# Performance work log

Measured on AMD Instinct MI355X. Metric: run time of the kernel, lower is better.

The kernel has to match this reference:

```python
import jax, jax.numpy as jnp
import numpy as np

B, N, NEV, E, D, L = 4, 20000, 100000, 400000, 64, 3

def setup_inputs() -> dict:
    key = jax.random.key(0)
    ks = jax.random.split(key, 12)
    x = jax.random.normal(ks[0], (B, N, 3), dtype=jnp.float32)
    # channel 0 is the susceptible boolean mask (0/1)
    mask0 = (jax.random.uniform(ks[1], (B, N)) < 0.3).astype(jnp.float32)
    x = x.at[..., 0].set(mask0)
    dag_edge_index = jax.random.randint(ks[2], (2, E), 0, NEV, dtype=jnp.int64)
    event_to_node = jax.random.randint(ks[3], (NEV,), 0, N, dtype=jnp.int64)
    event_src_node = jax.random.randint(ks[4], (NEV,), 0, N, dtype=jnp.int64)
    s = 1.0 / np.sqrt(D)
    Wp = jax.random.normal(ks[5], (6, D), dtype=jnp.float32) * (1.0 / np.sqrt(6))
    bp = jnp.zeros((D,), dtype=jnp.float32)
    Ws = jax.random.normal(ks[6], (L, D, D), dtype=jnp.float32) * s
    Wa = jax.random.normal(ks[7], (L, D, D), dtype=jnp.float32) * s
    ba = jnp.zeros((L, D), dtype=jnp.float32)
    Wo = jax.random.normal(ks[8], (D,), dtype=jnp.float32) * s
    bo = jnp.zeros((), dtype=jnp.float32)
    return {"x": x, "Wp": Wp, "bp": bp, "Ws": Ws, "Wa": Wa, "ba": ba,
            "Wo": Wo, "bo": bo, "dag_edge_index": dag_edge_index,
            "event_to_node": event_to_node, "event_src_node": event_src_node}

def reference(x, Wp, bp, Ws, Wa, ba, Wo, bo, dag_edge_index, event_to_node, event_src_node):
    n_events = event_src_node.shape[0]
    # event features: [B, n_events, 6] -> project -> ReLU
    ev_feat = jnp.concatenate([x[:, event_src_node, :], x[:, event_to_node, :]], axis=-1)
    h = jax.nn.relu(ev_feat @ Wp + bp)  # [B, n_events, D]
    # reversed DAG edges: src = dag[1], dst = dag[0]
    src_e, dst_e = dag_edge_index[1], dag_edge_index[0]
    deg = jnp.zeros((n_events,), h.dtype).at[dst_e].add(1.0)
    deg = jnp.maximum(deg, 1.0)[None, :, None]
    for l in range(Ws.shape[0]):
        agg = jnp.zeros_like(h).at[:, dst_e].add(h[:, src_e])  # scatter-add mean agg
        h = jax.nn.relu(h @ Ws[l] + (agg / deg) @ Wa[l] + ba[l])
    # aggregate events back to nodes (mean)
    node_emb = jnp.zeros((x.shape[0], x.shape[1], h.shape[-1]), h.dtype).at[:, event_to_node].add(h)
    count = jnp.zeros((x.shape[1],), h.dtype).at[event_to_node].add(1.0)
    node_emb = node_emb / jnp.maximum(count, 1.0)[None, :, None]
    scores = node_emb @ Wo + bo  # [B, N]
    susceptible = x[..., 0] > 0
    scores = jnp.where(susceptible, -jnp.inf, scores)
    return jax.nn.log_softmax(scores, axis=-1)
```

## Files before the change

kernel.cpp:

```cpp
#include <hip/hip_runtime.h>
#include <hip/hip_bf16.h>
#include <math.h>

constexpr int B   = 4;
constexpr int N   = 20000;
constexpr int NEV = 100000;
constexpr int E   = 400000;
constexpr int D   = 64;
constexpr int L   = 3;
constexpr int XS  = 136;
constexpr int CAP = 32;
constexpr int CHUNK = 625;

typedef short  short8 __attribute__((ext_vector_type(8)));
typedef float  f32x4  __attribute__((ext_vector_type(4)));
typedef float  f32x2  __attribute__((ext_vector_type(2)));


__device__ inline unsigned short f2bu(float f) {
  union { __hip_bfloat16 b; unsigned short s; } u;
  u.b = __float2bfloat16(f);
  return u.s;
}
__device__ inline unsigned packbf(float lo, float hi) {
  return ((unsigned)f2bu(hi) << 16) | (unsigned)f2bu(lo);
}


__global__ void k_zero(float4* __restrict__ p, int n4) {
  int i = blockIdx.x * blockDim.x + threadIdx.x;
  if (i < n4) p[i] = make_float4(0.f, 0.f, 0.f, 0.f);
}

__global__ void k_prep(const int* __restrict__ dag,
                       int* __restrict__ cnt,
                       int* __restrict__ csrc,
                       const int* __restrict__ e2n,
                       int* __restrict__ ncount,
                       const float* __restrict__ Ws,
                       const float* __restrict__ Wa,
                       unsigned short* __restrict__ Wt) {
  int bid = blockIdx.x;
  if (bid < 1563) {
    int i = bid * 256 + threadIdx.x;
    if (i < E) {
      int dst = dag[i];
      int src = dag[E + i];
      int pos = atomicAdd(&cnt[dst], 1);
      if (pos < CAP) csrc[dst * CAP + pos] = src;
    }
  } else if (bid < 1954) {
    int i = (bid - 1563) * 256 + threadIdx.x;
    if (i < NEV) atomicAdd(&ncount[e2n[i]], 1);
  } else {
    int i = (bid - 1954) * 256 + threadIdx.x;
    int l = i >> 13;
    int r = i & 8191;
    int n = r >> 7;
    int s = r & 127;
    int sl = (s < 64) ? s : s - 64;
    int c  = (sl & 3) * 16 + (sl >> 2);
    float v = (s < 64) ? Ws[l * 4096 + c * 64 + n]
                       : Wa[l * 4096 + c * 64 + n];
    Wt[l * 8192 + n * 128 + s] = f2bu(v);
  }
}

__global__ __launch_bounds__(256) void k_proj(const float* __restrict__ x,
                                              const float* __restrict__ Wp,
                                              const float* __restrict__ bp,
                                              const int* __restrict__ esrc,
                                              const int* __restrict__ e2n,
                                              unsigned* __restrict__ h,
                                              float* __restrict__ nscore) {
  int gid = blockIdx.x * blockDim.x + threadIdx.x;
  if (gid < B * N) nscore[gid] = 0.f;
  int p   = gid & 15;
  int row = gid >> 4;
  int e   = row >> 2;
  int b   = row & 3;
  int sn = esrc[e], tn = e2n[e];
  const float* xs = x + (size_t)(b * N + sn) * 3;
  const float* xt = x + (size_t)(b * N + tn) * 3;
  float xv[6] = {xs[0], xs[1], xs[2], xt[0], xt[1], xt[2]};
  float a[4];
#pragma unroll
  for (int t = 0; t < 4; ++t) {
    int d = p + 16 * t;
    float acc = bp[d];
#pragma unroll
    for (int k = 0; k < 6; ++k) acc += xv[k] * Wp[k * 64 + d];
    a[t] = fmaxf(acc, 0.f);
  }
  int w = __builtin_amdgcn_cvt_pk_fp8_f32(a[0], a[1], 0, false);
  w     = __builtin_amdgcn_cvt_pk_fp8_f32(a[2], a[3], w, true);
  h[row * 16 + p] = (unsigned)w;
}

template <bool LAST>
__global__ __launch_bounds__(256, 8) void k_layer(
    const unsigned short* __restrict__ Wt,
    const float* __restrict__ ba,
    const float* __restrict__ Wo,
    const int* __restrict__ e2n,
    const int* __restrict__ cnt,
    const int* __restrict__ csrc,
    const unsigned char* __restrict__ h_in,
    unsigned char* __restrict__ h_out,
    float* __restrict__ nscore) {
  __shared__ unsigned short sX[64 * XS];
  const int tid  = threadIdx.x;
  const int wv   = tid >> 6, lane = tid & 63;
  const int e0   = blockIdx.x * 16;
  const int r0   = e0 * 4;

  const int qg = lane >> 4, sub = lane & 15;
  int vidx = csrc[(size_t)(e0 + wv * 4 + qg) * CAP + sub];
  int c_l  = cnt[e0 + wv * 4 + (lane & 3)];

  {
    uint4 v = *(const uint4*)(h_in + (size_t)r0 * 64 + tid * 16);
    int row = tid >> 2, ch = tid & 3;
    unsigned vv[4] = {v.x, v.y, v.z, v.w};
    unsigned out[8];
#pragma unroll
    for (int i = 0; i < 4; ++i) {
      f32x2 lo = __builtin_amdgcn_cvt_pk_f32_fp8((int)vv[i], false);
      f32x2 hi = __builtin_amdgcn_cvt_pk_f32_fp8((int)vv[i], true);
      out[2 * i]     = packbf(lo[0], lo[1]);
      out[2 * i + 1] = packbf(hi[0], hi[1]);
    }
    unsigned short* dst = sX + row * XS + ch * 16;
    *(uint4*)dst       = *(uint4*)&out[0];
    *(uint4*)(dst + 8) = *(uint4*)&out[4];
  }

#pragma unroll
  for (int ei = 0; ei < 4; ++ei) {
    int c = __shfl(c_l, ei, 64);
    int cc16 = min(c, 16);
    float a0 = 0.f, a1 = 0.f, a2 = 0.f, a3 = 0.f;
    int j = 0;
    for (; j + 3 < cc16; j += 4) {
      int s0 = __shfl(vidx, ei * 16 + j + 0, 64);
      int s1 = __shfl(vidx, ei * 16 + j + 1, 64);
      int s2 = __shfl(vidx, ei * 16 + j + 2, 64);
      int s3 = __shfl(vidx, ei * 16 + j + 3, 64);
      unsigned v0 = *(const unsigned*)(h_in + (size_t)s0 * 256 + lane * 4);
      unsigned v1 = *(const unsigned*)(h_in + (size_t)s1 * 256 + lane * 4);
      unsigned v2 = *(const unsigned*)(h_in + (size_t)s2 * 256 + lane * 4);
      unsigned v3 = *(const unsigned*)(h_in + (size_t)s3 * 256 + lane * 4);
      f32x2 l0 = __builtin_amdgcn_cvt_pk_f32_fp8((int)v0, false);
      f32x2 h0 = __builtin_amdgcn_cvt_pk_f32_fp8((int)v0, true);
      f32x2 l1 = __builtin_amdgcn_cvt_pk_f32_fp8((int)v1, false);
      f32x2 h1 = __builtin_amdgcn_cvt_pk_f32_fp8((int)v1, true);
      f32x2 l2 = __builtin_amdgcn_cvt_pk_f32_fp8((int)v2, false);
      f32x2 h2 = __builtin_amdgcn_cvt_pk_f32_fp8((int)v2, true);
      f32x2 l3 = __builtin_amdgcn_cvt_pk_f32_fp8((int)v3, false);
      f32x2 h3 = __builtin_amdgcn_cvt_pk_f32_fp8((int)v3, true);
      a0 += l0[0] + l1[0] + l2[0] + l3[0];
      a1 += l0[1] + l1[1] + l2[1] + l3[1];
      a2 += h0[0] + h1[0] + h2[0] + h3[0];
      a3 += h0[1] + h1[1] + h2[1] + h3[1];
    }
    for (; j < cc16; ++j) {
      int s = __shfl(vidx, ei * 16 + j, 64);
      unsigned v = *(const unsigned*)(h_in + (size_t)s * 256 + lane * 4);
      f32x2 lo = __builtin_amdgcn_cvt_pk_f32_fp8((int)v, false);
      f32x2 hi = __builtin_amdgcn_cvt_pk_f32_fp8((int)v, true);
      a0 += lo[0]; a1 += lo[1]; a2 += hi[0]; a3 += hi[1];
    }
    int cc = min(c, CAP);
    for (int j2 = 16; j2 < cc; ++j2) {
      int s = csrc[(size_t)(e0 + wv * 4 + ei) * CAP + j2];
      unsigned v = *(const unsigned*)(h_in + (size_t)s * 256 + lane * 4);
      f32x2 lo = __builtin_amdgcn_cvt_pk_f32_fp8((int)v, false);
      f32x2 hi = __builtin_amdgcn_cvt_pk_f32_fp8((int)v, true);
      a0 += lo[0]; a1 += lo[1]; a2 += hi[0]; a3 += hi[1];
    }
    float inv = 1.f / fmaxf((float)c, 1.f);
    int lrow = (wv * 4 + ei) * 4 + qg;
    uint2 w;
    w.x = packbf(a0 * inv, a1 * inv);
    w.y = packbf(a2 * inv, a3 * inv);
    *(uint2*)(sX + lrow * XS + 64 + sub * 4) = w;
  }
  __syncthreads();

  const int m = lane & 15, q = lane >> 4;
  f32x4 acc[4];
#pragma unroll
  for (int t = 0; t < 4; ++t) {
    float bv = ba[t * 16 + m];
    acc[t] = (f32x4){bv, bv, bv, bv};
  }
  const unsigned short* xbase = sX + (wv * 16 + m) * XS + q * 8;
  const unsigned short* wbase = Wt + m * 128 + q * 8;
#pragma unroll
  for (int kk = 0; kk < 4; ++kk) {
    short8 av = *(const short8*)(xbase + kk * 32);
#pragma unroll
    for (int t = 0; t < 4; ++t) {
      short8 bv = *(const short8*)(wbase + t * 2048 + kk * 32);
      acc[t] = __builtin_amdgcn_mfma_f32_16x16x32_bf16(av, bv, acc[t], 0, 0, 0);
    }
  }

  if constexpr (!LAST) {
#pragma unroll
    for (int r = 0; r < 4; ++r) {
      int w = __builtin_amdgcn_cvt_pk_fp8_f32(fmaxf(acc[0][r], 0.f),
                                              fmaxf(acc[1][r], 0.f), 0, false);
      w     = __builtin_amdgcn_cvt_pk_fp8_f32(fmaxf(acc[2][r], 0.f),
                                              fmaxf(acc[3][r], 0.f), w, true);
      int grow = r0 + wv * 16 + q * 4 + r;
      ((unsigned*)h_out)[grow * 16 + m] = (unsigned)w;
    }
  } else {
    float w0 = Wo[m], w1 = Wo[16 + m], w2 = Wo[32 + m], w3 = Wo[48 + m];
#pragma unroll
    for (int r = 0; r < 4; ++r) {
      float v = fmaxf(acc[0][r], 0.f) * w0 + fmaxf(acc[1][r], 0.f) * w1
              + fmaxf(acc[2][r], 0.f) * w2 + fmaxf(acc[3][r], 0.f) * w3;
      v += __shfl_xor(v, 1, 64);
      v += __shfl_xor(v, 2, 64);
      v += __shfl_xor(v, 4, 64);
      v += __shfl_xor(v, 8, 64);
      if (m == 0) {
        int grow = r0 + wv * 16 + q * 4 + r;
        int e = grow >> 2, b = grow & 3;
        atomicAdd(&nscore[b * N + e2n[e]], v);
      }
    }
  }
}

__device__ inline float ls_score(const float* nscore, const int* ncount,
                                 const float* x, float bov, int b, int n) {
  return (x[(size_t)(b * N + n) * 3] > 0.f)
             ? -INFINITY
             : nscore[b * N + n] / fmaxf((float)ncount[n], 1.f) + bov;
}

__global__ __launch_bounds__(256) void k_ls1(const float* __restrict__ nscore,
                                             const int* __restrict__ ncount,
                                             const float* __restrict__ x,
                                             const float* __restrict__ bo,
                                             float* __restrict__ pmax,
                                             float* __restrict__ psum) {
  const int b = blockIdx.x >> 5, ch = blockIdx.x & 31;
  const int n0 = ch * CHUNK;
  const int tid = threadIdx.x;
  const float bov = bo[0];
  float s0 = -INFINITY, s1 = -INFINITY, s2 = -INFINITY;
  if (tid < CHUNK)       s0 = ls_score(nscore, ncount, x, bov, b, n0 + tid);
  if (tid + 256 < CHUNK) s1 = ls_score(nscore, ncount, x, bov, b, n0 + tid + 256);
  if (tid + 512 < CHUNK) s2 = ls_score(nscore, ncount, x, bov, b, n0 + tid + 512);
  float m = fmaxf(fmaxf(s0, s1), s2);
  __shared__ float red[4];
#pragma unroll
  for (int o = 32; o; o >>= 1) m = fmaxf(m, __shfl_xor(m, o, 64));
  if ((tid & 63) == 0) red[tid >> 6] = m;
  __syncthreads();
  float pm = fmaxf(fmaxf(red[0], red[1]), fmaxf(red[2], red[3]));
  float pm2 = (pm == -INFINITY) ? 0.f : pm;
  float e = expf(s0 - pm2) + expf(s1 - pm2) + expf(s2 - pm2);
#pragma unroll
  for (int o = 32; o; o >>= 1) e += __shfl_xor(e, o, 64);
  __syncthreads();
  if ((tid & 63) == 0) red[tid >> 6] = e;
  __syncthreads();
  if (tid == 0) {
    pmax[blockIdx.x] = pm;
    psum[blockIdx.x] = red[0] + red[1] + red[2] + red[3];
  }
}

__global__ __launch_bounds__(256) void k_ls3(const float* __restrict__ pmax,
                                             const float* __restrict__ psum,
                                             const float* __restrict__ nscore,
                                             const int* __restrict__ ncount,
                                             const float* __restrict__ x,
                                             const float* __restrict__ bo,
                                             float* __restrict__ out) {
  const int b = blockIdx.x >> 5, ch = blockIdx.x & 31;
  const int n0 = ch * CHUNK;
  const int tid = threadIdx.x;
  const float bov = bo[0];
  __shared__ float sgm, slse;
  if (tid < 64) {
    float pm = (tid < 32) ? pmax[b * 32 + tid] : -INFINITY;
    float ps = (tid < 32) ? psum[b * 32 + tid] : 0.f;
    float gm = pm;
#pragma unroll
    for (int o = 32; o; o >>= 1) gm = fmaxf(gm, __shfl_xor(gm, o, 64));
    float gm2 = (gm == -INFINITY) ? 0.f : gm;
    float c = (pm == -INFINITY) ? 0.f : ps * expf(pm - gm2);
#pragma unroll
    for (int o = 32; o; o >>= 1) c += __shfl_xor(c, o, 64);
    if (tid == 0) { sgm = gm; slse = logf(c); }
  }
  __syncthreads();
  const float gm = sgm, lse = slse;
  for (int i = tid; i < CHUNK; i += 256) {
    int n = n0 + i;
    float s = ls_score(nscore, ncount, x, bov, b, n);
    out[b * N + n] = fmaxf(s - gm - lse, -3.0e38f);
  }
}

extern "C" void kernel_launch(void* const* d_in, const int* in_sizes, int n_in,
                              void* d_out, int out_size, void* d_ws, size_t ws_size,
                              hipStream_t stream) {
  const float* x   = (const float*)d_in[0];
  const float* Wp  = (const float*)d_in[1];
  const float* bp  = (const float*)d_in[2];
  const float* Ws  = (const float*)d_in[3];
  const float* Wa  = (const float*)d_in[4];
  const float* ba  = (const float*)d_in[5];
  const float* Wo  = (const float*)d_in[6];
  const float* bo  = (const float*)d_in[7];
  const int*   dag = (const int*)d_in[8];
  const int*   e2n = (const int*)d_in[9];
  const int*   esr = (const int*)d_in[10];

  int*   ws     = (int*)d_ws;
  int*   cnt    = ws;
  int*   ncount = ws + 100000;
  float* nscore = (float*)(ws + 120000);
  float* pmax   = (float*)(ws + 200000);
  float* psum   = (float*)(ws + 200128);
  int*   csrc   = ws + 200704;
  unsigned short* Wt = (unsigned short*)(ws + 3400704);
  unsigned char* h0 = (unsigned char*)(ws + 3406912);
  unsigned char* h1 = h0 + (size_t)B * NEV * D;
  float* out    = (float*)d_out;

  k_zero<<<(30000 + 255) / 256, 256, 0, stream>>>((float4*)ws, 30000);
  k_prep<<<2050, 256, 0, stream>>>(dag, cnt, csrc, e2n, ncount, Ws, Wa, Wt);
  k_proj<<<(B * NEV * 16) / 256, 256, 0, stream>>>(x, Wp, bp, esr, e2n,
                                                   (unsigned*)h0, nscore);

  k_layer<false><<<NEV / 16, 256, 0, stream>>>(Wt,         ba,       Wo, e2n,
                                               cnt, csrc, h0, h1, nscore);
  k_layer<false><<<NEV / 16, 256, 0, stream>>>(Wt + 8192,  ba + D,   Wo, e2n,
                                               cnt, csrc, h1, h0, nscore);
  k_layer<true><<<NEV / 16, 256, 0, stream>>>(Wt + 16384,  ba + 2*D, Wo, e2n,
                                              cnt, csrc, h0, h1, nscore);

  k_ls1<<<B * 32, 256, 0, stream>>>(nscore, ncount, x, bo, pmax, psum);
  k_ls3<<<B * 32, 256, 0, stream>>>(pmax, psum, nscore, ncount, x, bo, out);
}
```

Measured before the change: 344.3 us.

## Batch neighbor gathers into register buffer and share event inputs via shuffles

In the layer kernel, the neighbor aggregation now issues all up-to-16 fp8 row gathers into a register buffer before any conversion or accumulation, so more loads are in flight at once instead of four at a time. In the projection kernel, each wavefront handles one event across all four batches: 24 lanes load the six input features per batch and broadcast them with shuffles, which removes redundant per-thread index and x loads. The risks are higher register pressure from the 16-entry buffer under launch_bounds(256,8), and predicated unrolled code.

```diff
diff --git a/kernel.cpp b/kernel.cpp
--- a/kernel.cpp
+++ b/kernel.cpp
@@ -75,14 +75,19 @@
                                               float* __restrict__ nscore) {
   int gid = blockIdx.x * blockDim.x + threadIdx.x;
   if (gid < B * N) nscore[gid] = 0.f;
-  int p   = gid & 15;
-  int row = gid >> 4;
-  int e   = row >> 2;
-  int b   = row & 3;
+  const int lane = threadIdx.x & 63;
+  const int e    = gid >> 6;
   int sn = esrc[e], tn = e2n[e];
-  const float* xs = x + (size_t)(b * N + sn) * 3;
-  const float* xt = x + (size_t)(b * N + tn) * 3;
-  float xv[6] = {xs[0], xs[1], xs[2], xt[0], xt[1], xt[2]};
+  float xval = 0.f;
+  if (lane < 24) {
+    int bl = lane / 6, rem = lane % 6;
+    int node = (rem < 3) ? sn : tn;
+    xval = x[(size_t)(bl * N + node) * 3 + (rem < 3 ? rem : rem - 3)];
+  }
+  const int b = lane >> 4, p = lane & 15;
+  float xv[6];
+#pragma unroll
+  for (int k = 0; k < 6; ++k) xv[k] = __shfl(xval, b * 6 + k, 64);
   float a[4];
 #pragma unroll
   for (int t = 0; t < 4; ++t) {
@@ -94,7 +99,7 @@
   }
   int w = __builtin_amdgcn_cvt_pk_fp8_f32(a[0], a[1], 0, false);
   w     = __builtin_amdgcn_cvt_pk_fp8_f32(a[2], a[3], w, true);
-  h[row * 16 + p] = (unsigned)w;
+  h[e * 64 + lane] = (unsigned)w;
 }
 
 template <bool LAST>
@@ -139,36 +144,22 @@
   for (int ei = 0; ei < 4; ++ei) {
     int c = __shfl(c_l, ei, 64);
     int cc16 = min(c, 16);
+    unsigned vbuf[16];
+#pragma unroll
+    for (int j = 0; j < 16; ++j) {
+      if (j < cc16) {
+        int s = __shfl(vidx, ei * 16 + j, 64);
+        vbuf[j] = *(const unsigned*)(h_in + (size_t)s * 256 + lane * 4);
+      }
+    }
     float a0 = 0.f, a1 = 0.f, a2 = 0.f, a3 = 0.f;
-    int j = 0;
-    for (; j + 3 < cc16; j += 4) {
-      int s0 = __shfl(vidx, ei * 16 + j + 0, 64);
-      int s1 = __shfl(vidx, ei * 16 + j + 1, 64);
-      int s2 = __shfl(vidx, ei * 16 + j + 2, 64);
-      int s3 = __shfl(vidx, ei * 16 + j + 3, 64);
-      unsigned v0 = *(const unsigned*)(h_in + (size_t)s0 * 256 + lane * 4);
-      unsigned v1 = *(const unsigned*)(h_in + (size_t)s1 * 256 + lane * 4);
-      unsigned v2 = *(const unsigned*)(h_in + (size_t)s2 * 256 + lane * 4);
-      unsigned v3 = *(const unsigned*)(h_in + (size_t)s3 * 256 + lane * 4);
-      f32x2 l0 = __builtin_amdgcn_cvt_pk_f32_fp8((int)v0, false);
-      f32x2 h0 = __builtin_amdgcn_cvt_pk_f32_fp8((int)v0, true);
-      f32x2 l1 = __builtin_amdgcn_cvt_pk_f32_fp8((int)v1, false);
-      f32x2 h1 = __builtin_amdgcn_cvt_pk_f32_fp8((int)v1, true);
-      f32x2 l2 = __builtin_amdgcn_cvt_pk_f32_fp8((int)v2, false);
-      f32x2 h2 = __builtin_amdgcn_cvt_pk_f32_fp8((int)v2, true);
-      f32x2 l3 = __builtin_amdgcn_cvt_pk_f32_fp8((int)v3, false);
-      f32x2 h3 = __builtin_amdgcn_cvt_pk_f32_fp8((int)v3, true);
-      a0 += l0[0] + l1[0] + l2[0] + l3[0];
-      a1 += l0[1] + l1[1] + l2[1] + l3[1];
-      a2 += h0[0] + h1[0] + h2[0] + h3[0];
-      a3 += h0[1] + h1[1] + h2[1] + h3[1];
-    }
-    for (; j < cc16; ++j) {
-      int s = __shfl(vidx, ei * 16 + j, 64);
-      unsigned v = *(const unsigned*)(h_in + (size_t)s * 256 + lane * 4);
-      f32x2 lo = __builtin_amdgcn_cvt_pk_f32_fp8((int)v, false);
-      f32x2 hi = __builtin_amdgcn_cvt_pk_f32_fp8((int)v, true);
-      a0 += lo[0]; a1 += lo[1]; a2 += hi[0]; a3 += hi[1];
+#pragma unroll
+    for (int j = 0; j < 16; ++j) {
+      if (j < cc16) {
+        f32x2 lo = __builtin_amdgcn_cvt_pk_f32_fp8((int)vbuf[j], false);
+        f32x2 hi = __builtin_amdgcn_cvt_pk_f32_fp8((int)vbuf[j], true);
+        a0 += lo[0]; a1 += lo[1]; a2 += hi[0]; a3 += hi[1];
+      }
     }
     int cc = min(c, CAP);
     for (int j2 = 16; j2 < cc; ++j2) {
```

Result: slower. 376.9 us (+9.4%).
